# Performance work log

Hardware: AMD Instinct MI355X
Metric: run time of the kernel (lower is better)

The kernel has to match this reference:

```python
import jax, jax.numpy as jnp
import numpy as np

EMBED = 1024
HEAD = 128

def setup_inputs() -> dict:
    key = jax.random.key(0)
    k1, k2, k3, k4 = jax.random.split(key, 4)
    x = jax.random.normal(k1, (4, 4096, EMBED), dtype=jnp.float32)
    # nn.Linear default init ~ U(-1/sqrt(fan_in), 1/sqrt(fan_in)); weights stored as [in, out] for x @ W
    s = 1.0 / np.sqrt(EMBED)
    Wq = jax.random.uniform(k2, (EMBED, HEAD), dtype=jnp.float32, minval=-s, maxval=s)
    Wk = jax.random.uniform(k3, (EMBED, HEAD), dtype=jnp.float32, minval=-s, maxval=s)
    Wv = jax.random.uniform(k4, (EMBED, HEAD), dtype=jnp.float32, minval=-s, maxval=s)
    return {"x": x, "Wq": Wq, "Wk": Wk, "Wv": Wv}

def reference(x, Wq, Wk, Wv):
    # x: [B, S, E]
    B, S, E = x.shape
    q = x @ Wq  # [B, S, H]
    k = x @ Wk
    v = x @ Wv
    scale = jnp.asarray(k.shape[-1], x.dtype) ** -0.5
    scores = jnp.einsum('bqh,bkh->bqk', q, k) * scale  # [B, S, S]
    causal = jnp.tril(jnp.ones((S, S), dtype=bool))
    scores = jnp.where(causal, scores, jnp.asarray(-jnp.inf, x.dtype))
    attn = jax.nn.softmax(scores, axis=-1)
    return jnp.einsum('bqk,bkh->bqh', attn, v)  # [B, S, H]
```

## Files before the change

kernel.cpp:

```cpp
#include <hip/hip_runtime.h>
#include <math.h>

#define BATCH 4
#define SEQ   4096
#define EMB   1024
#define HD    128
#define MROWS (BATCH*SEQ)
#define SCALE  0.08838834764831844f
#define SCALEQ 0.12751742f
#define CHUNK 10
#define NJOBS 119
#define MAXC  7

typedef __attribute__((ext_vector_type(8))) short bf16x8;
typedef __attribute__((ext_vector_type(4))) short short4v;
typedef __attribute__((ext_vector_type(4))) float f32x4;
typedef __attribute__((ext_vector_type(4))) int   i32x4;

static __device__ __forceinline__ unsigned short f2bf(float f) {
    unsigned int u = __float_as_uint(f);
    u += 0x7fff + ((u >> 16) & 1);
    return (unsigned short)(u >> 16);
}
static __device__ __forceinline__ float bf2f(unsigned short s) {
    return __uint_as_float((unsigned int)s << 16);
}
static __device__ __forceinline__ short4v pack4(float4 a) {
    short4v p;
    p[0] = (short)f2bf(a.x); p[1] = (short)f2bf(a.y);
    p[2] = (short)f2bf(a.z); p[3] = (short)f2bf(a.w);
    return p;
}

__global__ __launch_bounds__(256) void wtrans_kernel(
    const float* __restrict__ Wq, const float* __restrict__ Wk,
    const float* __restrict__ Wv, unsigned short* __restrict__ Wt)
{
    __shared__ __align__(16) unsigned short Xs[16 * 132];
    const int w  = blockIdx.y;
    const float* W = (w == 0) ? Wq : (w == 1) ? Wk : Wv;
    const float sc = (w == 0) ? SCALEQ : 1.0f;
    const int bx = blockIdx.x;
    const int k0 = bx * 16;
    const int t  = threadIdx.x;

#pragma unroll
    for (int i = 0; i < 2; ++i) {
        int gg = i * 256 + t;
        int row = gg >> 5, c4 = gg & 31;
        float4 a = *(const float4*)&W[(size_t)(k0 + row) * HD + c4 * 4];
        short4v p;
        p[0] = (short)f2bf(a.x * sc); p[1] = (short)f2bf(a.y * sc);
        p[2] = (short)f2bf(a.z * sc); p[3] = (short)f2bf(a.w * sc);
        *(short4v*)&Xs[row * 132 + c4 * 4] = p;
    }
    __syncthreads();
    const int n = t >> 1, g = t & 1;
    i32x4 o;
#pragma unroll
    for (int e = 0; e < 4; ++e) {
        unsigned int lo = Xs[(g * 8 + e * 2    ) * 132 + n];
        unsigned int hi = Xs[(g * 8 + e * 2 + 1) * 132 + n];
        o[e] = (int)(lo | (hi << 16));
    }
    const int ntg  = w * 8 + (n >> 4);
    const int kc   = bx >> 1;
    const int quad = (bx * 2 + g) & 3;
    const int lane = quad * 16 + (n & 15);
    *(i32x4*)&Wt[(((size_t)ntg * 32 + kc) * 64 + lane) * 8] = o;
}

__global__ __launch_bounds__(512, 2) void qkv_kernel(
    const float* __restrict__ x, const unsigned short* __restrict__ Wt,
    unsigned short* __restrict__ qb, unsigned short* __restrict__ kb,
    unsigned short* __restrict__ vtb)
{
    __shared__ __align__(16) unsigned short lds[26624];
    unsigned short* xs0 = lds;
    unsigned short* xs1 = lds + 4608;

    const int t    = threadIdx.x;
    const int lane = t & 63, ng = t >> 6;
    const int quad = lane >> 4, l16 = lane & 15;
    const int m0   = blockIdx.x * 64;

    f32x4 acc[4][3];
#pragma unroll
    for (int i = 0; i < 4; ++i)
#pragma unroll
        for (int j = 0; j < 3; ++j) acc[i][j] = (f32x4){0.f, 0.f, 0.f, 0.f};

    const int xr0 = t >> 4,        xs0c = (t & 15) * 4;
    const int xr1 = (t + 512) >> 4, xs1c = ((t + 512) & 15) * 4;
    const float* xb0 = x + (size_t)(m0 + xr0) * EMB + xs0c;
    const float* xb1 = x + (size_t)(m0 + xr1) * EMB + xs1c;

    const unsigned short* Wl = Wt + (size_t)lane * 8;
    const size_t jb0 = (size_t)(ng * 3 + 0) * 16384;
    const size_t jb1 = (size_t)(ng * 3 + 1) * 16384;
    const size_t jb2 = (size_t)(ng * 3 + 2) * 16384;

    bf16x8 aB0[2][3], aB1[2][3];
    float4 xra, xrb;

    {
        float4 a = *(const float4*)&xb0[0];
        float4 b = *(const float4*)&xb1[0];
#pragma unroll
        for (int ks = 0; ks < 2; ++ks) {
            aB0[ks][0] = *(const bf16x8*)&Wl[jb0 + (size_t)ks * 512];
            aB0[ks][1] = *(const bf16x8*)&Wl[jb1 + (size_t)ks * 512];
            aB0[ks][2] = *(const bf16x8*)&Wl[jb2 + (size_t)ks * 512];
        }
        *(short4v*)&xs0[xr0 * 72 + xs0c] = pack4(a);
        *(short4v*)&xs0[xr1 * 72 + xs1c] = pack4(b);
        xra = *(const float4*)&xb0[64];
        xrb = *(const float4*)&xb1[64];
    }
    asm volatile("s_waitcnt lgkmcnt(0)" ::: "memory");
    __builtin_amdgcn_s_barrier();

    for (int kt = 0; kt < EMB; kt += 128) {
        const size_t kcA = (size_t)(kt >> 5);
        *(short4v*)&xs1[xr0 * 72 + xs0c] = pack4(xra);
        *(short4v*)&xs1[xr1 * 72 + xs1c] = pack4(xrb);
        if (kt + 128 < EMB) {
            xra = *(const float4*)&xb0[kt + 128];
            xrb = *(const float4*)&xb1[kt + 128];
        }
#pragma unroll
        for (int ks = 0; ks < 2; ++ks) {
            aB1[ks][0] = *(const bf16x8*)&Wl[jb0 + (kcA + 2 + ks) * 512];
            aB1[ks][1] = *(const bf16x8*)&Wl[jb1 + (kcA + 2 + ks) * 512];
            aB1[ks][2] = *(const bf16x8*)&Wl[jb2 + (kcA + 2 + ks) * 512];
        }
        {
            bf16x8 aA[2][4];
#pragma unroll
            for (int ks = 0; ks < 2; ++ks)
#pragma unroll
                for (int mt = 0; mt < 4; ++mt)
                    aA[ks][mt] = *(const bf16x8*)&xs0[(mt * 16 + l16) * 72 + ks * 32 + quad * 8];
            __builtin_amdgcn_s_setprio(1);
#pragma unroll
            for (int ks = 0; ks < 2; ++ks)
#pragma unroll
                for (int mt = 0; mt < 4; ++mt)
#pragma unroll
                    for (int jt = 0; jt < 3; ++jt)
                        acc[mt][jt] = __builtin_amdgcn_mfma_f32_16x16x32_bf16(
                            aA[ks][mt], aB0[ks][jt], acc[mt][jt], 0, 0, 0);
            __builtin_amdgcn_s_setprio(0);
        }
        asm volatile("s_waitcnt lgkmcnt(0)" ::: "memory");
        __builtin_amdgcn_s_barrier();

        if (kt + 128 < EMB) {
            *(short4v*)&xs0[xr0 * 72 + xs0c] = pack4(xra);
            *(short4v*)&xs0[xr1 * 72 + xs1c] = pack4(xrb);
            if (kt + 192 < EMB) {
                xra = *(const float4*)&xb0[kt + 192];
                xrb = *(const float4*)&xb1[kt + 192];
            }
#pragma unroll
            for (int ks = 0; ks < 2; ++ks) {
                aB0[ks][0] = *(const bf16x8*)&Wl[jb0 + (kcA + 4 + ks) * 512];
                aB0[ks][1] = *(const bf16x8*)&Wl[jb1 + (kcA + 4 + ks) * 512];
                aB0[ks][2] = *(const bf16x8*)&Wl[jb2 + (kcA + 4 + ks) * 512];
            }
        }
        {
            bf16x8 aA[2][4];
#pragma unroll
            for (int ks = 0; ks < 2; ++ks)
#pragma unroll
                for (int mt = 0; mt < 4; ++mt)
                    aA[ks][mt] = *(const bf16x8*)&xs1[(mt * 16 + l16) * 72 + ks * 32 + quad * 8];
            __builtin_amdgcn_s_setprio(1);
#pragma unroll
            for (int ks = 0; ks < 2; ++ks)
#pragma unroll
                for (int mt = 0; mt < 4; ++mt)
#pragma unroll
                    for (int jt = 0; jt < 3; ++jt)
                        acc[mt][jt] = __builtin_amdgcn_mfma_f32_16x16x32_bf16(
                            aA[ks][mt], aB1[ks][jt], acc[mt][jt], 0, 0, 0);
            __builtin_amdgcn_s_setprio(0);
        }
        asm volatile("s_waitcnt lgkmcnt(0)" ::: "memory");
        __builtin_amdgcn_s_barrier();
    }

    unsigned short* Cq = lds;
    unsigned short* Ck = lds + 64 * 136;
    unsigned short* Cv = lds + 2 * 64 * 136;
#pragma unroll
    for (int mt = 0; mt < 4; ++mt)
#pragma unroll
        for (int jt = 0; jt < 3; ++jt) {
            int nt = ng * 3 + jt;
            int wm = nt >> 3, nl = nt & 7;
            if (wm < 2) {
                unsigned short* C = (wm == 0) ? Cq : Ck;
#pragma unroll
                for (int rr = 0; rr < 4; ++rr)
                    C[(mt * 16 + quad * 4 + rr) * 136 + nl * 16 + l16] =
                        f2bf(acc[mt][jt][rr]);
            } else {
                short4v p;
                p[0] = (short)f2bf(acc[mt][jt][0]); p[1] = (short)f2bf(acc[mt][jt][1]);
                p[2] = (short)f2bf(acc[mt][jt][2]); p[3] = (short)f2bf(acc[mt][jt][3]);
                *(short4v*)&Cv[(nl * 16 + l16) * 72 + mt * 16 + quad * 4] = p;
            }
        }
    __syncthreads();
    {
#pragma unroll
        for (int i = 0; i < 2; ++i) {
            int idx = i * 512 + t;
            int row = idx >> 4, seg = idx & 15;
            *(i32x4*)&qb[((size_t)(m0 + row)) * HD + seg * 8] = *(const i32x4*)&Cq[row * 136 + seg * 8];
            *(i32x4*)&kb[((size_t)(m0 + row)) * HD + seg * 8] = *(const i32x4*)&Ck[row * 136 + seg * 8];
        }
    }
    {
        const int b = m0 >> 12, s0 = m0 & 4095;
#pragma unroll
        for (int i = 0; i < 2; ++i) {
            int idx = i * 512 + t;
            int h = idx >> 3, seg = idx & 7;
            *(i32x4*)&vtb[(size_t)b * (HD * SEQ) + (size_t)h * SEQ + s0 + seg * 8] =
                *(const i32x4*)&Cv[h * 72 + seg * 8];
        }
    }
}

#define PADK 136
#define PADV 72
#define PADP 72
#define DEFER_THR 8.0f

__global__ __launch_bounds__(512, 4) void flash_kernel(
    const unsigned short* __restrict__ qb, const unsigned short* __restrict__ kb,
    const unsigned short* __restrict__ vtb, unsigned short* __restrict__ Opart,
    float* __restrict__ mbuf, float* __restrict__ lbuf)
{
    __shared__ __align__(16) unsigned short Ks[64 * PADK];
    __shared__ __align__(16) unsigned short Vt[128 * PADV];
    __shared__ __align__(16) unsigned short Pt[128 * PADP];

    const int bx   = blockIdx.x;
    const int slot = bx & 7, pp = bx >> 3;
    const int b    = slot >> 1;
    const int jj   = pp * 2 + (slot & 1);
    if (jj >= NJOBS) return;

    const int t    = threadIdx.x;
    const int lane = t & 63, w = t >> 6;
    const int quad = lane >> 4, l16 = lane & 15;

    int qi = 0, s = 0;
    for (qi = 0; qi < 32; ++qi) {
        int cnt = (qi + 5) / 5;
        if (jj < s + cnt) break;
        s += cnt;
    }
    const int c    = jj - s;
    const int qrow = qi * 128 + w * 16 + l16;
    const int jmax = 2 * qi + 2;
    const int jbeg = c * CHUNK;
    const int jend = min(jbeg + CHUNK, jmax);
    const int wtop = qi * 128 + w * 16;

    bf16x8 qf[4];
    {
        const unsigned short* qp = qb + ((size_t)b * SEQ + qrow) * HD;
#pragma unroll
        for (int ks = 0; ks < 4; ++ks)
            qf[ks] = *(const bf16x8*)&qp[ks * 32 + quad * 8];
    }

    f32x4 O[8];
#pragma unroll
    for (int i = 0; i < 8; ++i) O[i] = (f32x4){0.f, 0.f, 0.f, 0.f};
    float m_run = -1e30f, l_run = 0.f;

    const unsigned short* kbb  = kb  + (size_t)b * SEQ * HD;
    const unsigned short* vtbb = vtb + (size_t)b * HD * SEQ;

    const int gg0 = t, gg1 = 512 + t;
    i32x4 kr0, kr1, vr0, vr1;
    kr0 = *(const i32x4*)&kbb[(size_t)jbeg * 64 * HD + (size_t)gg0 * 8];
    kr1 = *(const i32x4*)&kbb[(size_t)jbeg * 64 * HD + (size_t)gg1 * 8];
    vr0 = *(const i32x4*)&vtbb[(size_t)(gg0 >> 3) * SEQ + jbeg * 64 + (gg0 & 7) * 8];
    vr1 = *(const i32x4*)&vtbb[(size_t)(gg1 >> 3) * SEQ + jbeg * 64 + (gg1 & 7) * 8];

    for (int j0 = jbeg; j0 < jend; ++j0) {
        __syncthreads();
        *(i32x4*)&Ks[(gg0 >> 4) * PADK + (gg0 & 15) * 8] = kr0;
        *(i32x4*)&Ks[(gg1 >> 4) * PADK + (gg1 & 15) * 8] = kr1;
        *(i32x4*)&Vt[(gg0 >> 3) * PADV + (gg0 & 7) * 8] = vr0;
        *(i32x4*)&Vt[(gg1 >> 3) * PADV + (gg1 & 7) * 8] = vr1;
        __syncthreads();

        if (j0 + 1 < jend) {
            const int j1 = j0 + 1;
            kr0 = *(const i32x4*)&kbb[(size_t)j1 * 64 * HD + (size_t)gg0 * 8];
            kr1 = *(const i32x4*)&kbb[(size_t)j1 * 64 * HD + (size_t)gg1 * 8];
            vr0 = *(const i32x4*)&vtbb[(size_t)(gg0 >> 3) * SEQ + j1 * 64 + (gg0 & 7) * 8];
            vr1 = *(const i32x4*)&vtbb[(size_t)(gg1 >> 3) * SEQ + j1 * 64 + (gg1 & 7) * 8];
        }

        if (j0 * 64 > wtop + 15) continue;

        f32x4 st[4];
        __builtin_amdgcn_s_setprio(1);
#pragma unroll
        for (int mt = 0; mt < 4; ++mt) {
            f32x4 a = (f32x4){0.f, 0.f, 0.f, 0.f};
#pragma unroll
            for (int ks = 0; ks < 4; ++ks) {
                bf16x8 kf = *(const bf16x8*)&Ks[(mt * 16 + l16) * PADK + ks * 32 + quad * 8];
                a = __builtin_amdgcn_mfma_f32_16x16x32_bf16(kf, qf[ks], a, 0, 0, 0);
            }
            st[mt] = a;
        }
        __builtin_amdgcn_s_setprio(0);

        if (j0 * 64 + 63 > wtop) {
#pragma unroll
            for (int mt = 0; mt < 4; ++mt)
#pragma unroll
                for (int rr = 0; rr < 4; ++rr) {
                    int kv = j0 * 64 + mt * 16 + quad * 4 + rr;
                    if (kv > qrow) st[mt][rr] = -1e30f;
                }
        }

        float mx = -1e30f;
#pragma unroll
        for (int mt = 0; mt < 4; ++mt)
#pragma unroll
            for (int rr = 0; rr < 4; ++rr) mx = fmaxf(mx, st[mt][rr]);
        mx = fmaxf(mx, __shfl_xor(mx, 16));
        mx = fmaxf(mx, __shfl_xor(mx, 32));
        if (!__all(mx <= m_run + DEFER_THR)) {
            const float m_new = fmaxf(m_run, mx);
            const float alpha = exp2f(m_run - m_new);
            l_run *= alpha;
#pragma unroll
            for (int i = 0; i < 8; ++i) {
                O[i][0] *= alpha; O[i][1] *= alpha; O[i][2] *= alpha; O[i][3] *= alpha;
            }
            m_run = m_new;
        }
        float psum = 0.f;
#pragma unroll
        for (int mt = 0; mt < 4; ++mt)
#pragma unroll
            for (int rr = 0; rr < 4; ++rr) {
                float p = exp2f(st[mt][rr] - m_run);
                st[mt][rr] = p;
                psum += p;
            }
        psum += __shfl_xor(psum, 16);
        psum += __shfl_xor(psum, 32);
        l_run += psum;

#pragma unroll
        for (int mt = 0; mt < 4; ++mt) {
            short4v p;
            p[0] = (short)f2bf(st[mt][0]); p[1] = (short)f2bf(st[mt][1]);
            p[2] = (short)f2bf(st[mt][2]); p[3] = (short)f2bf(st[mt][3]);
            *(short4v*)&Pt[(w * 16 + l16) * PADP + mt * 16 + quad * 4] = p;
        }

        bf16x8 pf0 = *(const bf16x8*)&Pt[(w * 16 + l16) * PADP + quad * 8];
        bf16x8 pf1 = *(const bf16x8*)&Pt[(w * 16 + l16) * PADP + 32 + quad * 8];
        __builtin_amdgcn_s_setprio(1);
#pragma unroll
        for (int mt = 0; mt < 8; ++mt) {
            bf16x8 vf0 = *(const bf16x8*)&Vt[(mt * 16 + l16) * PADV + quad * 8];
            bf16x8 vf1 = *(const bf16x8*)&Vt[(mt * 16 + l16) * PADV + 32 + quad * 8];
            O[mt] = __builtin_amdgcn_mfma_f32_16x16x32_bf16(vf0, pf0, O[mt], 0, 0, 0);
            O[mt] = __builtin_amdgcn_mfma_f32_16x16x32_bf16(vf1, pf1, O[mt], 0, 0, 0);
        }
        __builtin_amdgcn_s_setprio(0);
    }

    const int r = w * 16 + l16;
    const size_t jobbase = (size_t)b * NJOBS + jj;
    unsigned short* po = Opart + jobbase * (128 * 128) + (size_t)r * 128;
#pragma unroll
    for (int mt = 0; mt < 8; ++mt) {
        short4v p;
        p[0] = (short)f2bf(O[mt][0]); p[1] = (short)f2bf(O[mt][1]);
        p[2] = (short)f2bf(O[mt][2]); p[3] = (short)f2bf(O[mt][3]);
        *(short4v*)&po[mt * 16 + quad * 4] = p;
    }
    if (quad == 0) {
        mbuf[jobbase * 128 + r] = m_run;
        lbuf[jobbase * 128 + r] = l_run;
    }
}

__global__ __launch_bounds__(512) void combine_kernel(
    const unsigned short* __restrict__ Opart, const float* __restrict__ mbuf,
    const float* __restrict__ lbuf, float* __restrict__ out)
{
    const int qi = blockIdx.x, b = blockIdx.y;
    const int nc = (qi + 5) / 5;
    int j0 = 0;
    for (int q = 0; q < qi; ++q) j0 += (q + 5) / 5;
    const int t = threadIdx.x;
    const int row = t >> 2, cg = (t & 3) * 32;

    float mv[MAXC], lv[MAXC];
    float M = -1e30f;
#pragma unroll
    for (int c2 = 0; c2 < MAXC; ++c2) {
        if (c2 < nc) {
            const size_t jb = (size_t)b * NJOBS + j0 + c2;
            mv[c2] = mbuf[jb * 128 + row];
            lv[c2] = lbuf[jb * 128 + row];
            M = fmaxf(M, mv[c2]);
        } else { mv[c2] = -1e30f; lv[c2] = 0.f; }
    }
    float L = 0.f;
#pragma unroll
    for (int c2 = 0; c2 < MAXC; ++c2)
        if (c2 < nc) L += exp2f(mv[c2] - M) * lv[c2];
    const float Linv = 1.0f / L;

    float acc[32];
#pragma unroll
    for (int i = 0; i < 32; ++i) acc[i] = 0.f;
#pragma unroll
    for (int c2 = 0; c2 < MAXC; ++c2) {
        if (c2 < nc) {
            const float wgt = exp2f(mv[c2] - M) * Linv;
            const unsigned short* po = Opart + ((size_t)b * NJOBS + j0 + c2) * (128 * 128) +
                                       (size_t)row * 128 + cg;
#pragma unroll
            for (int i = 0; i < 4; ++i) {
                i32x4 d = *(const i32x4*)&po[i * 8];
#pragma unroll
                for (int e = 0; e < 4; ++e) {
                    unsigned int u = (unsigned int)d[e];
                    acc[i * 8 + e * 2]     = fmaf(wgt, bf2f((unsigned short)(u & 0xffff)), acc[i * 8 + e * 2]);
                    acc[i * 8 + e * 2 + 1] = fmaf(wgt, bf2f((unsigned short)(u >> 16)),   acc[i * 8 + e * 2 + 1]);
                }
            }
        }
    }
    float* op = out + ((size_t)b * SEQ + qi * 128 + row) * HD + cg;
#pragma unroll
    for (int i = 0; i < 8; ++i) {
        float4 res;
        res.x = acc[i * 4]; res.y = acc[i * 4 + 1];
        res.z = acc[i * 4 + 2]; res.w = acc[i * 4 + 3];
        *(float4*)&op[i * 4] = res;
    }
}

extern "C" void kernel_launch(void* const* d_in, const int* in_sizes, int n_in,
                              void* d_out, int out_size, void* d_ws, size_t ws_size,
                              hipStream_t stream) {
    const float* x  = (const float*)d_in[0];
    const float* Wq = (const float*)d_in[1];
    const float* Wk = (const float*)d_in[2];
    const float* Wv = (const float*)d_in[3];

    unsigned short* qb    = (unsigned short*)d_ws;
    unsigned short* kb    = qb  + (size_t)MROWS * HD;
    unsigned short* vtb   = kb  + (size_t)MROWS * HD;
    unsigned short* Wt    = vtb + (size_t)MROWS * HD;
    unsigned short* Opart = Wt  + (size_t)3 * HD * EMB;
    float* mbuf = (float*)(Opart + (size_t)BATCH * NJOBS * 128 * 128);
    float* lbuf = mbuf + (size_t)BATCH * NJOBS * 128;
    float* out = (float*)d_out;

    wtrans_kernel <<<dim3(64, 3),  dim3(256), 0, stream>>>(Wq, Wk, Wv, Wt);
    qkv_kernel    <<<dim3(256),    dim3(512), 0, stream>>>(x, Wt, qb, kb, vtb);
    flash_kernel  <<<dim3(480),    dim3(512), 0, stream>>>(qb, kb, vtb, Opart, mbuf, lbuf);
    combine_kernel<<<dim3(32, 4),  dim3(512), 0, stream>>>(Opart, mbuf, lbuf, out);
}
```

Baseline: 171.5 us.

## Stage QKV weights through LDS via direct global-to-LDS loads, use hardware bf16 pack

The QKV projection kernel now streams weight tiles straight into a double-buffered LDS region with global_load_lds, instead of holding them in registers loaded from global memory. The two-step unrolled k-loop becomes a 16-phase ping-pong loop with a vmcnt wait and a barrier each phase. Separately, the software float-to-bf16 rounding is replaced with the v_cvt_pk_bf16_f32 instruction in several epilogues and in the P-tile packing of the attention kernel. The larger LDS footprint (about 114 KB) may limit the 2-blocks-per-CU occupancy, and the new loop has more barriers.

```diff
diff --git a/kernel.cpp b/kernel.cpp
--- a/kernel.cpp
+++ b/kernel.cpp
@@ -16,6 +16,7 @@
 typedef __attribute__((ext_vector_type(4))) short short4v;
 typedef __attribute__((ext_vector_type(4))) float f32x4;
 typedef __attribute__((ext_vector_type(4))) int   i32x4;
+typedef __attribute__((ext_vector_type(2))) int   i32x2;
 
 static __device__ __forceinline__ unsigned short f2bf(float f) {
     unsigned int u = __float_as_uint(f);
@@ -30,6 +31,16 @@
     p[0] = (short)f2bf(a.x); p[1] = (short)f2bf(a.y);
     p[2] = (short)f2bf(a.z); p[3] = (short)f2bf(a.w);
     return p;
+}
+static __device__ __forceinline__ int cvtpk(float lo, float hi) {
+    int r;
+    asm("v_cvt_pk_bf16_f32 %0, %1, %2" : "=v"(r) : "v"(lo), "v"(hi));
+    return r;
+}
+static __device__ __forceinline__ void gload_lds16(const unsigned short* g, unsigned short* l) {
+    __builtin_amdgcn_global_load_lds(
+        (const __attribute__((address_space(1))) void*)g,
+        (__attribute__((address_space(3))) void*)l, 16, 0, 0);
 }
 
 __global__ __launch_bounds__(256) void wtrans_kernel(
@@ -75,9 +86,10 @@
     unsigned short* __restrict__ qb, unsigned short* __restrict__ kb,
     unsigned short* __restrict__ vtb)
 {
-    __shared__ __align__(16) unsigned short lds[26624];
-    unsigned short* xs0 = lds;
-    unsigned short* xs1 = lds + 4608;
+    __shared__ __align__(1024) unsigned short lds[58368];
+    unsigned short* Ws  = lds;
+    unsigned short* xsA = lds + 49152;
+    unsigned short* xsB = lds + 53760;
 
     const int t    = threadIdx.x;
     const int lane = t & 63, ng = t >> 6;
@@ -90,57 +102,67 @@
 #pragma unroll
         for (int j = 0; j < 3; ++j) acc[i][j] = (f32x4){0.f, 0.f, 0.f, 0.f};
 
-    const int xr0 = t >> 4,        xs0c = (t & 15) * 4;
-    const int xr1 = (t + 512) >> 4, xs1c = ((t + 512) & 15) * 4;
-    const float* xb0 = x + (size_t)(m0 + xr0) * EMB + xs0c;
-    const float* xb1 = x + (size_t)(m0 + xr1) * EMB + xs1c;
-
-    const unsigned short* Wl = Wt + (size_t)lane * 8;
-    const size_t jb0 = (size_t)(ng * 3 + 0) * 16384;
-    const size_t jb1 = (size_t)(ng * 3 + 1) * 16384;
-    const size_t jb2 = (size_t)(ng * 3 + 2) * 16384;
-
-    bf16x8 aB0[2][3], aB1[2][3];
+    const int xr0 = t >> 4,         xc0 = (t & 15) * 4;
+    const int xr1 = (t + 512) >> 4, xc1 = ((t + 512) & 15) * 4;
+    const float* xb0 = x + (size_t)(m0 + xr0) * EMB + xc0;
+    const float* xb1 = x + (size_t)(m0 + xr1) * EMB + xc1;
+
+    const unsigned short* Wg = Wt + (size_t)lane * 8;
     float4 xra, xrb;
 
     {
         float4 a = *(const float4*)&xb0[0];
         float4 b = *(const float4*)&xb1[0];
-#pragma unroll
-        for (int ks = 0; ks < 2; ++ks) {
-            aB0[ks][0] = *(const bf16x8*)&Wl[jb0 + (size_t)ks * 512];
-            aB0[ks][1] = *(const bf16x8*)&Wl[jb1 + (size_t)ks * 512];
-            aB0[ks][2] = *(const bf16x8*)&Wl[jb2 + (size_t)ks * 512];
-        }
-        *(short4v*)&xs0[xr0 * 72 + xs0c] = pack4(a);
-        *(short4v*)&xs0[xr1 * 72 + xs1c] = pack4(b);
+        *(short4v*)&xsA[xr0 * 72 + xc0] = pack4(a);
+        *(short4v*)&xsA[xr1 * 72 + xc1] = pack4(b);
+#pragma unroll
+        for (int jt = 0; jt < 3; ++jt)
+#pragma unroll
+            for (int kcl = 0; kcl < 2; ++kcl) {
+                int ntg = ng * 3 + jt;
+                gload_lds16(Wg + ((size_t)ntg * 32 + kcl) * 512,
+                            Ws + ((size_t)ntg * 2 + kcl) * 512);
+            }
         xra = *(const float4*)&xb0[64];
         xrb = *(const float4*)&xb1[64];
     }
+    asm volatile("s_waitcnt vmcnt(2)" ::: "memory");
     asm volatile("s_waitcnt lgkmcnt(0)" ::: "memory");
     __builtin_amdgcn_s_barrier();
 
-    for (int kt = 0; kt < EMB; kt += 128) {
-        const size_t kcA = (size_t)(kt >> 5);
-        *(short4v*)&xs1[xr0 * 72 + xs0c] = pack4(xra);
-        *(short4v*)&xs1[xr1 * 72 + xs1c] = pack4(xrb);
-        if (kt + 128 < EMB) {
-            xra = *(const float4*)&xb0[kt + 128];
-            xrb = *(const float4*)&xb1[kt + 128];
-        }
-#pragma unroll
-        for (int ks = 0; ks < 2; ++ks) {
-            aB1[ks][0] = *(const bf16x8*)&Wl[jb0 + (kcA + 2 + ks) * 512];
-            aB1[ks][1] = *(const bf16x8*)&Wl[jb1 + (kcA + 2 + ks) * 512];
-            aB1[ks][2] = *(const bf16x8*)&Wl[jb2 + (kcA + 2 + ks) * 512];
-        }
+    for (int ph = 0; ph < 16; ++ph) {
+        const int cb = ph & 1, nb = cb ^ 1;
+        unsigned short* xc = cb ? xsB : xsA;
+        unsigned short* xn = cb ? xsA : xsB;
+        const int kcn = (ph < 15 ? ph + 1 : 15) * 2;
+
+#pragma unroll
+        for (int jt = 0; jt < 3; ++jt)
+#pragma unroll
+            for (int kcl = 0; kcl < 2; ++kcl) {
+                int ntg = ng * 3 + jt;
+                gload_lds16(Wg + ((size_t)ntg * 32 + kcn + kcl) * 512,
+                            Ws + ((size_t)(nb * 48) + ntg * 2 + kcl) * 512);
+            }
+        *(short4v*)&xn[xr0 * 72 + xc0] = pack4(xra);
+        *(short4v*)&xn[xr1 * 72 + xc1] = pack4(xrb);
         {
-            bf16x8 aA[2][4];
+            const int xcol = (ph + 2 < 16) ? (ph + 2) * 64 : 960;
+            xra = *(const float4*)&xb0[xcol];
+            xrb = *(const float4*)&xb1[xcol];
+        }
+        {
+            bf16x8 aA[2][4], aB[2][3];
 #pragma unroll
             for (int ks = 0; ks < 2; ++ks)
 #pragma unroll
+                for (int jt = 0; jt < 3; ++jt)
+                    aB[ks][jt] = *(const bf16x8*)&Ws[((size_t)(cb * 48) + (ng * 3 + jt) * 2 + ks) * 512 + lane * 8];
+#pragma unroll
+            for (int ks = 0; ks < 2; ++ks)
+#pragma unroll
                 for (int mt = 0; mt < 4; ++mt)
-                    aA[ks][mt] = *(const bf16x8*)&xs0[(mt * 16 + l16) * 72 + ks * 32 + quad * 8];
+                    aA[ks][mt] = *(const bf16x8*)&xc[(mt * 16 + l16) * 72 + ks * 32 + quad * 8];
             __builtin_amdgcn_s_setprio(1);
 #pragma unroll
             for (int ks = 0; ks < 2; ++ks)
@@ -149,44 +171,10 @@
 #pragma unroll
                     for (int jt = 0; jt < 3; ++jt)
                         acc[mt][jt] = __builtin_amdgcn_mfma_f32_16x16x32_bf16(
-                            aA[ks][mt], aB0[ks][jt], acc[mt][jt], 0, 0, 0);
+                            aA[ks][mt], aB[ks][jt], acc[mt][jt], 0, 0, 0);
             __builtin_amdgcn_s_setprio(0);
         }
-        asm volatile("s_waitcnt lgkmcnt(0)" ::: "memory");
-        __builtin_amdgcn_s_barrier();
-
-        if (kt + 128 < EMB) {
-            *(short4v*)&xs0[xr0 * 72 + xs0c] = pack4(xra);
-            *(short4v*)&xs0[xr1 * 72 + xs1c] = pack4(xrb);
-            if (kt + 192 < EMB) {
-                xra = *(const float4*)&xb0[kt + 192];
-                xrb = *(const float4*)&xb1[kt + 192];
-            }
-#pragma unroll
-            for (int ks = 0; ks < 2; ++ks) {
-                aB0[ks][0] = *(const bf16x8*)&Wl[jb0 + (kcA + 4 + ks) * 512];
-                aB0[ks][1] = *(const bf16x8*)&Wl[jb1 + (kcA + 4 + ks) * 512];
-                aB0[ks][2] = *(const bf16x8*)&Wl[jb2 + (kcA + 4 + ks) * 512];
-            }
-        }
-        {
-            bf16x8 aA[2][4];
-#pragma unroll
-            for (int ks = 0; ks < 2; ++ks)
-#pragma unroll
-                for (int mt = 0; mt < 4; ++mt)
-                    aA[ks][mt] = *(const bf16x8*)&xs1[(mt * 16 + l16) * 72 + ks * 32 + quad * 8];
-            __builtin_amdgcn_s_setprio(1);
-#pragma unroll
-            for (int ks = 0; ks < 2; ++ks)
-#pragma unroll
-                for (int mt = 0; mt < 4; ++mt)
-#pragma unroll
-                    for (int jt = 0; jt < 3; ++jt)
-                        acc[mt][jt] = __builtin_amdgcn_mfma_f32_16x16x32_bf16(
-                            aA[ks][mt], aB1[ks][jt], acc[mt][jt], 0, 0, 0);
-            __builtin_amdgcn_s_setprio(0);
-        }
+        asm volatile("s_waitcnt vmcnt(2)" ::: "memory");
         asm volatile("s_waitcnt lgkmcnt(0)" ::: "memory");
         __builtin_amdgcn_s_barrier();
     }
@@ -207,10 +195,10 @@
                     C[(mt * 16 + quad * 4 + rr) * 136 + nl * 16 + l16] =
                         f2bf(acc[mt][jt][rr]);
             } else {
-                short4v p;
-                p[0] = (short)f2bf(acc[mt][jt][0]); p[1] = (short)f2bf(acc[mt][jt][1]);
-                p[2] = (short)f2bf(acc[mt][jt][2]); p[3] = (short)f2bf(acc[mt][jt][3]);
-                *(short4v*)&Cv[(nl * 16 + l16) * 72 + mt * 16 + quad * 4] = p;
+                i32x2 p;
+                p[0] = cvtpk(acc[mt][jt][0], acc[mt][jt][1]);
+                p[1] = cvtpk(acc[mt][jt][2], acc[mt][jt][3]);
+                *(i32x2*)&Cv[(nl * 16 + l16) * 72 + mt * 16 + quad * 4] = p;
             }
         }
     __syncthreads();
@@ -369,10 +357,10 @@
 
 #pragma unroll
         for (int mt = 0; mt < 4; ++mt) {
-            short4v p;
-            p[0] = (short)f2bf(st[mt][0]); p[1] = (short)f2bf(st[mt][1]);
-            p[2] = (short)f2bf(st[mt][2]); p[3] = (short)f2bf(st[mt][3]);
-            *(short4v*)&Pt[(w * 16 + l16) * PADP + mt * 16 + quad * 4] = p;
+            i32x2 p;
+            p[0] = cvtpk(st[mt][0], st[mt][1]);
+            p[1] = cvtpk(st[mt][2], st[mt][3]);
+            *(i32x2*)&Pt[(w * 16 + l16) * PADP + mt * 16 + quad * 4] = p;
         }
 
         bf16x8 pf0 = *(const bf16x8*)&Pt[(w * 16 + l16) * PADP + quad * 8];
@@ -393,10 +381,10 @@
     unsigned short* po = Opart + jobbase * (128 * 128) + (size_t)r * 128;
 #pragma unroll
     for (int mt = 0; mt < 8; ++mt) {
-        short4v p;
-        p[0] = (short)f2bf(O[mt][0]); p[1] = (short)f2bf(O[mt][1]);
-        p[2] = (short)f2bf(O[mt][2]); p[3] = (short)f2bf(O[mt][3]);
-        *(short4v*)&po[mt * 16 + quad * 4] = p;
+        i32x2 p;
+        p[0] = cvtpk(O[mt][0], O[mt][1]);
+        p[1] = cvtpk(O[mt][2], O[mt][3]);
+        *(i32x2*)&po[mt * 16 + quad * 4] = p;
     }
     if (quad == 0) {
         mbuf[jobbase * 128 + r] = m_run;
```

Measured after the change: 169.0 us. Within noise of the previous version (-1.5%).
